# Performance work log

Hardware: AMD Instinct MI355X
Metric: run time of the kernel (lower is better)

The kernel has to match this reference:

```python
import jax, jax.numpy as jnp
import numpy as np

B, H, W, C = 32, 64, 64, 512
NH, WH, WW = 16, 8, 8
SH, SW = 4, 4
FF = 2048
META = 384
A = WH * WW
EPS = 1e-5


def _rel_coords_log():
    # pairwise relative coords in log-space, shape (A*A, 2)
    coords = np.stack(np.meshgrid(np.arange(WH), np.arange(WW), indexing='ij')).reshape(2, -1)
    rel = coords[:, :, None] - coords[:, None, :]
    rel = rel.transpose(1, 2, 0).reshape(-1, 2).astype(np.float32)
    return np.sign(rel) * np.log1p(np.abs(rel))


def _attn_mask():
    # shifted-window attention mask, shape (nW, A, A)
    img = np.zeros((H, W), np.float32)
    cnt = 0
    for hs in (slice(0, -WH), slice(-WH, -SH), slice(-SH, None)):
        for ws in (slice(0, -WW), slice(-WW, -SW), slice(-SW, None)):
            img[hs, ws] = cnt
            cnt += 1
    mw = img.reshape(H // WH, WH, W // WW, WW).transpose(0, 2, 1, 3).reshape(-1, A)
    diff = mw[:, None, :] - mw[:, :, None]
    return np.where(diff != 0, -100.0, 0.0).astype(np.float32)


def setup_inputs():
    key = jax.random.key(0)
    ks = jax.random.split(key, 8)
    s = 0.02
    return {
        'x': jax.random.normal(ks[0], (B, H * W, C), jnp.float32),
        'qkv_w': jax.random.normal(ks[1], (C, 3 * C), jnp.float32) * s,
        'qkv_b': jnp.zeros((3 * C,), jnp.float32),
        'proj_w': jax.random.normal(ks[2], (C, C), jnp.float32) * s,
        'proj_b': jnp.zeros((C,), jnp.float32),
        'tau': jnp.ones((NH,), jnp.float32),
        'meta_w1': jax.random.normal(ks[3], (2, META), jnp.float32) * s,
        'meta_b1': jnp.zeros((META,), jnp.float32),
        'meta_w2': jax.random.normal(ks[4], (META, NH), jnp.float32) * s,
        'meta_b2': jnp.zeros((NH,), jnp.float32),
        'norm1_g': jnp.ones((C,), jnp.float32),
        'norm1_b': jnp.zeros((C,), jnp.float32),
        'norm2_g': jnp.ones((C,), jnp.float32),
        'norm2_b': jnp.zeros((C,), jnp.float32),
        'mlp_w1': jax.random.normal(ks[5], (C, FF), jnp.float32) * s,
        'mlp_b1': jnp.zeros((FF,), jnp.float32),
        'mlp_w2': jax.random.normal(ks[6], (FF, C), jnp.float32) * s,
        'mlp_b2': jnp.zeros((C,), jnp.float32),
    }


def _layernorm(x, g, b):
    mu = x.mean(-1, keepdims=True)
    var = ((x - mu) ** 2).mean(-1, keepdims=True)
    return (x - mu) * jax.lax.rsqrt(var + EPS) * g + b


def reference(x, qkv_w, qkv_b, proj_w, proj_b, tau, meta_w1, meta_b1, meta_w2, meta_b2,
              norm1_g, norm1_b, norm2_g, norm2_b, mlp_w1, mlp_b1, mlp_w2, mlp_b2):
    rel_log = jnp.asarray(_rel_coords_log())
    mask = jnp.asarray(_attn_mask())                 # (nW, A, A)
    nW = mask.shape[0]
    hd = C // NH

    # relative position bias from meta MLP (dropout inactive at eval)
    bias = jax.nn.relu(rel_log @ meta_w1 + meta_b1) @ meta_w2 + meta_b2  # (A*A, NH)
    bias = bias.T.reshape(NH, A, A)

    # cyclic shift + window partition
    xr = x.reshape(B, H, W, C)
    xr = jnp.roll(xr, (-SH, -SW), axis=(1, 2))
    xw = xr.reshape(B, H // WH, WH, W // WW, WW, C).transpose(0, 1, 3, 2, 4, 5)
    xw = xw.reshape(B * nW, A, C)

    qkv = (xw @ qkv_w + qkv_b).reshape(B * nW, A, 3, NH, hd).transpose(2, 0, 3, 1, 4)
    q, k, v = qkv[0], qkv[1], qkv[2]                 # (B*nW, NH, A, hd)

    qn = jnp.linalg.norm(q, axis=-1, keepdims=True)
    kn = jnp.linalg.norm(k, axis=-1, keepdims=True)
    denom = jnp.clip(qn * kn.transpose(0, 1, 3, 2), 1e-6, None)
    attn = jnp.einsum('wnid,wnjd->wnij', q, k) / denom
    attn = attn / jnp.clip(tau, 0.01, None).reshape(1, NH, 1, 1)
    attn = attn + bias[None]
    attn = attn.reshape(B, nW, NH, A, A) + mask[None, :, None]
    attn = jax.nn.softmax(attn.reshape(B * nW, NH, A, A), axis=-1)

    out = jnp.einsum('wnij,wnjd->wnid', attn, v)
    out = out.transpose(0, 2, 1, 3).reshape(B * nW, A, C)
    out = out @ proj_w + proj_b

    # window reverse + reverse shift
    out = out.reshape(B, H // WH, W // WW, WH, WW, C).transpose(0, 1, 3, 2, 4, 5).reshape(B, H, W, C)
    out = jnp.roll(out, (SH, SW), axis=(1, 2)).reshape(B, H * W, C)

    # swin-v2 post-norm residuals
    x = x + _layernorm(out, norm1_g, norm1_b)
    hmid = jax.nn.gelu(x @ mlp_w1 + mlp_b1, approximate=False) @ mlp_w2 + mlp_b2
    x = x + _layernorm(hmid, norm2_g, norm2_b)
    return x
```

## Files before the change

kernel.cpp:

```cpp
#include <hip/hip_runtime.h>

typedef unsigned short u16;
typedef __attribute__((ext_vector_type(8))) short     bf16x8;
typedef __attribute__((ext_vector_type(8))) unsigned short u16x8;
typedef __attribute__((ext_vector_type(4))) unsigned short u16x4;
typedef __attribute__((ext_vector_type(4))) float     f32x4;

#define GADDR(p) ((const __attribute__((address_space(1))) void*)(p))
#define LADDR(p) ((__attribute__((address_space(3))) void*)(p))

__device__ __forceinline__ u16 f2bf(float f) {
  unsigned u = __float_as_uint(f);
  u += 0x7fffu + ((u >> 16) & 1u);
  return (u16)(u >> 16);
}
__device__ __forceinline__ float bf2f(u16 h) {
  return __uint_as_float(((unsigned)h) << 16);
}

__global__ void wt_kernel(const float* __restrict__ w, u16* __restrict__ wt,
                          int K, int N) {
  size_t idx = (size_t)blockIdx.x * 256 + threadIdx.x;
  if (idx >= (size_t)K * N) return;
  int n = (int)(idx / K);
  int k = (int)(idx % K);
  wt[idx] = f2bf(w[(size_t)k * N + n]);
}

__global__ __launch_bounds__(64)
void bias_kernel(const float* __restrict__ w1, const float* __restrict__ b1,
                 const float* __restrict__ w2, const float* __restrict__ b2,
                 float* __restrict__ out) {
  const int p = blockIdx.x;
  const int i = p >> 6, j = p & 63;
  const float d0 = (float)((i >> 3) - (j >> 3));
  const float d1 = (float)((i & 7) - (j & 7));
  const float r0 = copysignf(log1pf(fabsf(d0)), d0);
  const float r1 = copysignf(log1pf(fabsf(d1)), d1);
  float part[16];
#pragma unroll
  for (int h = 0; h < 16; ++h) part[h] = 0.f;
  for (int m = threadIdx.x; m < 384; m += 64) {
    float hv = fmaxf(r0 * w1[m] + r1 * w1[384 + m] + b1[m], 0.f);
#pragma unroll
    for (int h = 0; h < 16; ++h) part[h] += hv * w2[m * 16 + h];
  }
#pragma unroll
  for (int h = 0; h < 16; ++h) {
    float v = part[h];
#pragma unroll
    for (int off = 32; off; off >>= 1) v += __shfl_xor(v, off);
    if (threadIdx.x == 0) out[(size_t)h * 4096 + p] = v + b2[h];
  }
}

__global__ __launch_bounds__(64)
void bias2_kernel(const float* __restrict__ bb, float* __restrict__ b2) {
  const int blk = blockIdx.x;
  const int h = blk >> 4, mi = (blk >> 2) & 3, ni = blk & 3;
  const int lane = threadIdx.x, fr = lane & 15, fq = lane >> 4;
  float4 o;
  o.x = bb[(size_t)h * 4096 + (mi * 16 + fq * 4 + 0) * 64 + ni * 16 + fr];
  o.y = bb[(size_t)h * 4096 + (mi * 16 + fq * 4 + 1) * 64 + ni * 16 + fr];
  o.z = bb[(size_t)h * 4096 + (mi * 16 + fq * 4 + 2) * 64 + ni * 16 + fr];
  o.w = bb[(size_t)h * 4096 + (mi * 16 + fq * 4 + 3) * 64 + ni * 16 + fr];
  ((float4*)b2)[(size_t)blk * 64 + lane] = o;
}

__global__ __launch_bounds__(512)
void partition_kernel(const float* __restrict__ x, u16* __restrict__ xw) {
  const size_t r = (size_t)blockIdx.x * 4 + (threadIdx.x >> 7);
  const int t = threadIdx.x & 127;
  const int w   = (int)(r >> 6);
  const int i   = (int)(r & 63);
  const int b   = w >> 6;
  const int win = w & 63;
  const int hs = (((win >> 3) << 3) + (i >> 3) + 4) & 63;
  const int ws2 = (((win & 7) << 3) + (i & 7) + 4) & 63;
  const float4* src = (const float4*)(x + (((size_t)b << 12) + hs * 64 + ws2) * 512);
  u16* dst = xw + r * 512;
  float4 v = src[t];
  u16x4 o;
  o[0] = f2bf(v.x); o[1] = f2bf(v.y); o[2] = f2bf(v.z); o[3] = f2bf(v.w);
  *(u16x4*)(dst + t * 4) = o;
}

template <int MODE>
__global__ __launch_bounds__(512, 1)
void gemm8(const u16* __restrict__ A, const u16* __restrict__ Wt,
           const float* __restrict__ bias, void* __restrict__ outp,
           int M, int N, int K) {
  __shared__ u16 lds[65536];
  const int t = threadIdx.x;
  const int gx = gridDim.x;
  const int nwg = gx * gridDim.y;
  const int wg = blockIdx.y * gx + blockIdx.x;
  const int swzb = (wg & 7) * (nwg >> 3) + (wg >> 3);
  const int n0 = (swzb % gx) * 256;
  const int m0 = (swzb / gx) * 256;

  const int lane = t & 63;
  const int wid = t >> 6;
  const int wr = (wid >> 2) * 128;
  const int wc = (wid & 3) * 64;
  const int fr = lane & 15, fq = lane >> 4;
  const int c0 = (fq ^ (fr & 7)) * 8;
  const int c1 = ((4 + fq) ^ (fr & 7)) * 8;

  const int tq = t >> 3;
  const int scol = ((t & 7) ^ (tq & 7)) * 8;
  const u16* Asrc = A  + (size_t)(m0 + tq) * K + scol;
  const int rowB = (tq & 31) + ((t >> 8) << 6);
  const u16* Bsrc = Wt + (size_t)(n0 + rowB) * K + scol;
  const int dA = t * 8;
  const int dB = 16384 + ((t >> 8) << 11) + t * 8;

#define SG_A(slot, src, h) do {                                               \
    const int _d = (slot) * 32768 + (h) * 4096 + dA;                          \
    const size_t _k = (size_t)(src) * 64 + (size_t)((h) * 64) * K;            \
    __builtin_amdgcn_global_load_lds(GADDR(Asrc + _k), LADDR(&lds[_d]), 16, 0, 0); \
    __builtin_amdgcn_global_load_lds(GADDR(Asrc + _k + (size_t)128 * K),      \
                                     LADDR(&lds[_d + 8192]), 16, 0, 0);       \
  } while (0)
#define SG_B(slot, src, h) do {                                               \
    const int _d = (slot) * 32768 + (h) * 2048 + dB;                          \
    const size_t _k = (size_t)(src) * 64 + (size_t)((h) * 32) * K;            \
    __builtin_amdgcn_global_load_lds(GADDR(Bsrc + _k), LADDR(&lds[_d]), 16, 0, 0); \
    __builtin_amdgcn_global_load_lds(GADDR(Bsrc + _k + (size_t)128 * K),      \
                                     LADDR(&lds[_d + 8192]), 16, 0, 0);       \
  } while (0)

  f32x4 acc[8][4];
#pragma unroll
  for (int a = 0; a < 8; ++a)
#pragma unroll
    for (int b = 0; b < 4; ++b) acc[a][b] = (f32x4){0.f, 0.f, 0.f, 0.f};

  const int NT = K >> 6;
  SG_A(0, 0, 0); SG_A(0, 0, 1); SG_B(0, 0, 0); SG_B(0, 0, 1);
  SG_A(1, 1, 0); SG_B(1, 1, 0); SG_B(1, 1, 1);
  asm volatile("s_waitcnt vmcnt(6)" ::: "memory");
  __builtin_amdgcn_s_barrier();

#define TILE_BODY(S, SLOT, NSLOT, P0_COND)                                    \
  {                                                                           \
    const u16* la = lds + (SLOT) * 32768;                                     \
    const u16* lb = la + 16384;                                               \
    bf16x8 af[8], bf0[4], bf1[4];                                             \
    _Pragma("unroll")                                                         \
    for (int mi = 0; mi < 4; ++mi) {                                          \
      const int r = (wr + mi * 16 + fr) * 64;                                 \
      af[mi * 2]     = *(const bf16x8*)&la[r + c0];                           \
      af[mi * 2 + 1] = *(const bf16x8*)&la[r + c1];                           \
    }                                                                         \
    _Pragma("unroll")                                                         \
    for (int ni = 0; ni < 2; ++ni) {                                          \
      const int r = (wc + ni * 16 + fr) * 64;                                 \
      bf0[ni * 2]     = *(const bf16x8*)&lb[r + c0];                          \
      bf0[ni * 2 + 1] = *(const bf16x8*)&lb[r + c1];                          \
    }                                                                         \
    if (P0_COND) SG_A(NSLOT, (S) + 1, 1);                                     \
    __builtin_amdgcn_s_barrier();                                             \
    asm volatile("s_waitcnt lgkmcnt(0)" ::: "memory");                        \
    __builtin_amdgcn_sched_barrier(0);                                        \
    __builtin_amdgcn_s_setprio(1);                                            \
    _Pragma("unroll")                                                         \
    for (int mi = 0; mi < 4; ++mi)                                            \
      _Pragma("unroll")                                                       \
      for (int ni = 0; ni < 2; ++ni) {                                        \
        acc[mi][ni] = __builtin_amdgcn_mfma_f32_16x16x32_bf16(                \
            af[mi * 2], bf0[ni * 2], acc[mi][ni], 0, 0, 0);                   \
        acc[mi][ni] = __builtin_amdgcn_mfma_f32_16x16x32_bf16(                \
            af[mi * 2 + 1], bf0[ni * 2 + 1], acc[mi][ni], 0, 0, 0);           \
      }                                                                       \
    __builtin_amdgcn_s_setprio(0);                                            \
    __builtin_amdgcn_s_barrier();                                             \
    _Pragma("unroll")                                                         \
    for (int ni = 0; ni < 2; ++ni) {                                          \
      const int r = (wc + 32 + ni * 16 + fr) * 64;                            \
      bf1[ni * 2]     = *(const bf16x8*)&lb[r + c0];                          \
      bf1[ni * 2 + 1] = *(const bf16x8*)&lb[r + c1];                          \
    }                                                                         \
    if ((S) + 2 < NT) SG_A(SLOT, (S) + 2, 0);                                 \
    __builtin_amdgcn_s_barrier();                                             \
    asm volatile("s_waitcnt lgkmcnt(0)" ::: "memory");                        \
    __builtin_amdgcn_sched_barrier(0);                                        \
    __builtin_amdgcn_s_setprio(1);                                            \
    _Pragma("unroll")                                                         \
    for (int mi = 0; mi < 4; ++mi)                                            \
      _Pragma("unroll")                                                       \
      for (int ni = 0; ni < 2; ++ni) {                                        \
        acc[mi][2 + ni] = __builtin_amdgcn_mfma_f32_16x16x32_bf16(            \
            af[mi * 2], bf1[ni * 2], acc[mi][2 + ni], 0, 0, 0);               \
        acc[mi][2 + ni] = __builtin_amdgcn_mfma_f32_16x16x32_bf16(            \
            af[mi * 2 + 1], bf1[ni * 2 + 1], acc[mi][2 + ni], 0, 0, 0);       \
      }                                                                       \
    __builtin_amdgcn_s_setprio(0);                                            \
    __builtin_amdgcn_s_barrier();                                             \
    _Pragma("unroll")                                                         \
    for (int mi = 0; mi < 4; ++mi) {                                          \
      const int r = (wr + 64 + mi * 16 + fr) * 64;                            \
      af[mi * 2]     = *(const bf16x8*)&la[r + c0];                           \
      af[mi * 2 + 1] = *(const bf16x8*)&la[r + c1];                           \
    }                                                                         \
    if ((S) + 2 < NT) SG_B(SLOT, (S) + 2, 0);                                 \
    __builtin_amdgcn_s_barrier();                                             \
    asm volatile("s_waitcnt lgkmcnt(0)" ::: "memory");                        \
    __builtin_amdgcn_sched_barrier(0);                                        \
    __builtin_amdgcn_s_setprio(1);                                            \
    _Pragma("unroll")                                                         \
    for (int mi = 0; mi < 4; ++mi)                                            \
      _Pragma("unroll")                                                       \
      for (int ni = 0; ni < 2; ++ni) {                                        \
        acc[4 + mi][ni] = __builtin_amdgcn_mfma_f32_16x16x32_bf16(            \
            af[mi * 2], bf0[ni * 2], acc[4 + mi][ni], 0, 0, 0);               \
        acc[4 + mi][ni] = __builtin_amdgcn_mfma_f32_16x16x32_bf16(            \
            af[mi * 2 + 1], bf0[ni * 2 + 1], acc[4 + mi][ni], 0, 0, 0);       \
      }                                                                       \
    __builtin_amdgcn_s_setprio(0);                                            \
    __builtin_amdgcn_s_barrier();                                             \
    if ((S) + 2 < NT) SG_B(SLOT, (S) + 2, 1);                                 \
    __builtin_amdgcn_s_barrier();                                             \
    __builtin_amdgcn_s_setprio(1);                                            \
    _Pragma("unroll")                                                         \
    for (int mi = 0; mi < 4; ++mi)                                            \
      _Pragma("unroll")                                                       \
      for (int ni = 0; ni < 2; ++ni) {                                        \
        acc[4 + mi][2 + ni] = __builtin_amdgcn_mfma_f32_16x16x32_bf16(        \
            af[mi * 2], bf1[ni * 2], acc[4 + mi][2 + ni], 0, 0, 0);           \
        acc[4 + mi][2 + ni] = __builtin_amdgcn_mfma_f32_16x16x32_bf16(        \
            af[mi * 2 + 1], bf1[ni * 2 + 1], acc[4 + mi][2 + ni], 0, 0, 0);   \
      }                                                                       \
    __builtin_amdgcn_s_setprio(0);                                            \
    if ((S) + 2 < NT) asm volatile("s_waitcnt vmcnt(6)" ::: "memory");        \
    else              asm volatile("s_waitcnt vmcnt(0)" ::: "memory");        \
    __builtin_amdgcn_s_barrier();                                             \
  }

  for (int s = 0; s < NT; s += 2) {
    TILE_BODY(s,     0, 1, true);
    TILE_BODY(s + 1, 1, 0, (s + 2 < NT));
  }
#undef TILE_BODY
#undef SG_A
#undef SG_B
  asm volatile("s_waitcnt vmcnt(0)" ::: "memory");
  __syncthreads();

  float bv4[4];
#pragma unroll
  for (int ni = 0; ni < 4; ++ni) bv4[ni] = bias[n0 + wc + ni * 16 + fr];

  u16* uW = &lds[wid * 8192];
  u16* og = (u16*)outp;
#pragma unroll
  for (int mi = 0; mi < 8; ++mi) {
#pragma unroll
    for (int ni = 0; ni < 4; ++ni)
#pragma unroll
      for (int j = 0; j < 4; ++j) {
        float v = acc[mi][ni][j] + bv4[ni];
        if (MODE == 2) {
          const float a2 = v * (1.5957691216f + 0.0713548162f * v * v);
          const float e = __expf(a2);
          v = v * (e * __builtin_amdgcn_rcpf(e + 1.0f));
        }
        uW[(fq * 4 + j) * 64 + ((ni ^ j ^ fq) & 3) * 16 + fr] = f2bf(v);
      }
#pragma unroll
    for (int p = 0; p < 2; ++p) {
      const int r = p * 8 + (lane >> 3);
      const int sg = (((lane & 7) >> 1) ^ (r & 3) ^ ((r >> 2) & 3)) & 3;
      u16x8 v8 = *(const u16x8*)&uW[r * 64 + sg * 16 + (lane & 1) * 8];
      const int row = m0 + wr + mi * 16 + r;
      *(u16x8*)&og[(size_t)row * N + n0 + wc + (lane & 7) * 8] = v8;
    }
  }
}

template <int LNM>
__global__ __launch_bounds__(512, 1)
void gemm_ln(const u16* __restrict__ A, const u16* __restrict__ Wt,
             const float* __restrict__ bias, const u16* __restrict__ residb,
             const float* __restrict__ g, const float* __restrict__ bt,
             float* __restrict__ out1, u16* __restrict__ out1b, int K) {
  __shared__ u16 lds[61440];
  const int t = threadIdx.x;
  const int nwg = gridDim.x;
  const int wg = blockIdx.x;
  const int swz = (wg & 7) * (nwg >> 3) + (wg >> 3);
  const int m0 = swz * 128;

  const int lane = t & 63;
  const int wid = t >> 6;
  const int wc = wid * 64;
  const int fr = lane & 15, fq = lane >> 4;
  const int rx = (fr >> 1) & 3;

  const int srow = t >> 2;
  const int schk = ((t & 3) ^ ((srow >> 1) & 3)) * 8;
  const u16* Ag = A  + (size_t)(m0 + srow) * K + schk;
  const u16* Bg = Wt + (size_t)srow * K + schk;

#define GLSTAGE_A(tile, buf)                                                  \
    __builtin_amdgcn_global_load_lds(GADDR(Ag + (size_t)(tile) * 32),         \
        LADDR(&lds[(buf) * 20480 + t * 8]), 16, 0, 0)
#define GLSTAGE_B(tile, buf, p)                                               \
    __builtin_amdgcn_global_load_lds(                                         \
        GADDR(Bg + (size_t)(p) * 128 * K + (size_t)(tile) * 32),              \
        LADDR(&lds[(buf) * 20480 + 4096 + (p) * 4096 + t * 8]), 16, 0, 0)

  f32x4 acc[8][4];
#pragma unroll
  for (int a = 0; a < 8; ++a)
#pragma unroll
    for (int b = 0; b < 4; ++b) acc[a][b] = (f32x4){0.f, 0.f, 0.f, 0.f};

  const int NT = K >> 5;
  GLSTAGE_A(0, 0);
  GLSTAGE_B(0, 0, 0); GLSTAGE_B(0, 0, 1); GLSTAGE_B(0, 0, 2); GLSTAGE_B(0, 0, 3);
  GLSTAGE_A(1, 1);
  GLSTAGE_B(1, 1, 0); GLSTAGE_B(1, 1, 1); GLSTAGE_B(1, 1, 2); GLSTAGE_B(1, 1, 3);

  int cur = 0;
  for (int u = 0; u < NT; ++u) {
    if (u + 1 < NT) asm volatile("s_waitcnt vmcnt(5)" ::: "memory");
    else            asm volatile("s_waitcnt vmcnt(0)" ::: "memory");
    __builtin_amdgcn_s_barrier();

    const u16* lb = lds + cur * 20480;
    const int stg = (cur == 0) ? 2 : cur - 1;
    bf16x8 bfr[4], af0[4], af1[4];
#pragma unroll
    for (int ni = 0; ni < 4; ++ni)
      bfr[ni] = *(const bf16x8*)&lb[4096 + (wc + ni * 16 + fr) * 32 + (fq ^ rx) * 8];
#pragma unroll
    for (int mi = 0; mi < 4; ++mi)
      af0[mi] = *(const bf16x8*)&lb[(mi * 16 + fr) * 32 + (fq ^ rx) * 8];
    if (u + 2 < NT) {
      GLSTAGE_A(u + 2, stg);
      GLSTAGE_B(u + 2, stg, 0); GLSTAGE_B(u + 2, stg, 1);
    }
#pragma unroll
    for (int mi = 0; mi < 4; ++mi)
      af1[mi] = *(const bf16x8*)&lb[((4 + mi) * 16 + fr) * 32 + (fq ^ rx) * 8];
    if (u + 2 < NT) {
      GLSTAGE_B(u + 2, stg, 2); GLSTAGE_B(u + 2, stg, 3);
    }

    __builtin_amdgcn_s_setprio(1);
#pragma unroll
    for (int mi = 0; mi < 4; ++mi)
#pragma unroll
      for (int ni = 0; ni < 4; ++ni)
        acc[mi][ni] = __builtin_amdgcn_mfma_f32_16x16x32_bf16(
            af0[mi], bfr[ni], acc[mi][ni], 0, 0, 0);
    __builtin_amdgcn_s_setprio(0);
    __builtin_amdgcn_s_setprio(1);
#pragma unroll
    for (int mi = 0; mi < 4; ++mi)
#pragma unroll
      for (int ni = 0; ni < 4; ++ni)
        acc[4 + mi][ni] = __builtin_amdgcn_mfma_f32_16x16x32_bf16(
            af1[mi], bfr[ni], acc[4 + mi][ni], 0, 0, 0);
    __builtin_amdgcn_s_setprio(0);
    cur = (cur == 2) ? 0 : cur + 1;
  }
#undef GLSTAGE_A
#undef GLSTAGE_B

  __syncthreads();
  float bv4[4];
#pragma unroll
  for (int ni = 0; ni < 4; ++ni) bv4[ni] = bias[wc + ni * 16 + fr];
  float4 ga = ((const float4*)g)[lane * 2];
  float4 gb = ((const float4*)g)[lane * 2 + 1];
  float4 ba = ((const float4*)bt)[lane * 2];
  float4 bb = ((const float4*)bt)[lane * 2 + 1];
  const float gv[8] = {ga.x, ga.y, ga.z, ga.w, gb.x, gb.y, gb.z, gb.w};
  const float bv[8] = {ba.x, ba.y, ba.z, ba.w, bb.x, bb.y, bb.z, bb.w};
  float* fLN = (float*)lds;

#pragma unroll
  for (int mi = 0; mi < 8; ++mi) {
#pragma unroll
    for (int ni = 0; ni < 4; ++ni)
#pragma unroll
      for (int j = 0; j < 4; ++j) {
        const int ch = ((wid * 4 + ni) ^ (j << 2) ^ fq) & 31;
        fLN[(fq * 4 + j) * 512 + ch * 16 + fr] = acc[mi][ni][j] + bv4[ni];
      }
    __syncthreads();
#pragma unroll
    for (int rr = 0; rr < 2; ++rr) {
      const int r = wid * 2 + rr;
      const int gci = lane >> 1;
      const int ch = (gci ^ ((r & 3) << 2) ^ (r >> 2)) & 31;
      const int base = r * 512 + ch * 16 + (lane & 1) * 8;
      f32x4 va = *(const f32x4*)&fLN[base];
      f32x4 vb = *(const f32x4*)&fLN[base + 4];
      float v[8] = {va[0], va[1], va[2], va[3], vb[0], vb[1], vb[2], vb[3]};
      float s = 0.f, s2 = 0.f;
#pragma unroll
      for (int e = 0; e < 8; ++e) { s += v[e]; s2 = fmaf(v[e], v[e], s2); }
#pragma unroll
      for (int off = 32; off; off >>= 1) {
        s += __shfl_xor(s, off); s2 += __shfl_xor(s2, off);
      }
      const float mu = s * (1.f / 512.f);
      const float rs = rsqrtf(s2 * (1.f / 512.f) - mu * mu + 1e-5f);
      const int rowg = m0 + mi * 16 + r;
      u16x8 rv8 = *(const u16x8*)(residb + (size_t)rowg * 512 + lane * 8);
      float rv[8];
#pragma unroll
      for (int e = 0; e < 8; ++e) rv[e] = bf2f(rv8[e]);
      float o[8];
#pragma unroll
      for (int e = 0; e < 8; ++e)
        o[e] = rv[e] + (v[e] - mu) * rs * gv[e] + bv[e];
      if (LNM == 0) {
        const int w = rowg >> 6, i = rowg & 63;
        const int b = w >> 6, win = w & 63;
        const int hs = (((win >> 3) << 3) + (i >> 3) + 4) & 63;
        const int ws2 = (((win & 7) << 3) + (i & 7) + 4) & 63;
        const size_t token = ((size_t)b << 12) + hs * 64 + ws2;
        u16x8 ob;
#pragma unroll
        for (int e = 0; e < 8; ++e) ob[e] = f2bf(o[e]);
        *(u16x8*)(out1b + token * 512 + lane * 8) = ob;
      } else {
        float* op = out1 + (size_t)rowg * 512 + lane * 8;
        ((f32x4*)op)[0] = (f32x4){o[0], o[1], o[2], o[3]};
        ((f32x4*)op)[1] = (f32x4){o[4], o[5], o[6], o[7]};
      }
    }
    __syncthreads();
  }
}

__global__ __launch_bounds__(64)
void attn_kernel(const u16* __restrict__ qkv, const float* __restrict__ bias2,
                 const float* __restrict__ tau, u16* __restrict__ ao) {
  const int h = blockIdx.x;
  const int w = blockIdx.y;
  const int lane = threadIdx.x;
  const int fr = lane & 15, fq = lane >> 4;

  __shared__ u16 sh[7424];

  const size_t rowb = ((size_t)w * 64 + lane) * 1536 + (size_t)h * 32;
  u16x8 q8[4], k8[4], v8[4];
#pragma unroll
  for (int u = 0; u < 4; ++u) {
    q8[u] = ((const u16x8*)(qkv + rowb))[u];
    k8[u] = ((const u16x8*)(qkv + rowb + 512))[u];
    v8[u] = ((const u16x8*)(qkv + rowb + 1024))[u];
  }
  float qv[32], kv[32];
  float qn = 0.f, kn = 0.f;
#pragma unroll
  for (int d = 0; d < 32; ++d) {
    qv[d] = bf2f(q8[d >> 3][d & 7]); qn = fmaf(qv[d], qv[d], qn);
    kv[d] = bf2f(k8[d >> 3][d & 7]); kn = fmaf(kv[d], kv[d], kn);
  }
  const float itau = 1.0f / fmaxf(tau[h], 0.01f);
  const float qs = rsqrtf(fmaxf(qn, 1e-24f)) * itau;
  const float ks = rsqrtf(fmaxf(kn, 1e-24f));
#pragma unroll
  for (int u = 0; u < 4; ++u) {
    u16x8 qo, ko;
#pragma unroll
    for (int e = 0; e < 8; ++e) {
      qo[e] = f2bf(qv[u * 8 + e] * qs);
      ko[e] = f2bf(kv[u * 8 + e] * ks);
    }
    *(u16x8*)&sh[lane * 40 + u * 8] = qo;
    *(u16x8*)&sh[2560 + lane * 40 + u * 8] = ko;
  }
#pragma unroll
  for (int d = 0; d < 32; ++d)
    sh[5120 + d * 72 + lane] = v8[d >> 3][d & 7];
  __syncthreads();

  f32x4 acc[4][4];
  const float4* b2 = (const float4*)bias2 + (size_t)h * 1024 + lane;
#pragma unroll
  for (int mi = 0; mi < 4; ++mi)
#pragma unroll
    for (int ni = 0; ni < 4; ++ni) {
      float4 bv = b2[(mi * 4 + ni) * 64];
      acc[mi][ni] = (f32x4){bv.x, bv.y, bv.z, bv.w};
    }
  const int win = w & 63, wh = win >> 3, ww = win & 7;
  if (wh == 7 || ww == 7) {
    int labc[4];
#pragma unroll
    for (int ni = 0; ni < 4; ++ni) {
      const int c = ni * 16 + fr;
      labc[ni] = ((wh == 7) ? (((c >> 3) < 4) ? 1 : 2) : 0) * 3
               + ((ww == 7) ? (((c & 7) < 4) ? 1 : 2) : 0);
    }
#pragma unroll
    for (int mi = 0; mi < 4; ++mi)
#pragma unroll
      for (int j = 0; j < 4; ++j) {
        const int r = mi * 16 + fq * 4 + j;
        const int lr = ((wh == 7) ? (((r >> 3) < 4) ? 1 : 2) : 0) * 3
                     + ((ww == 7) ? (((r & 7) < 4) ? 1 : 2) : 0);
#pragma unroll
        for (int ni = 0; ni < 4; ++ni)
          if (lr != labc[ni]) acc[mi][ni][j] -= 100.f;
      }
  }

  {
    bf16x8 af[4], bf[4];
#pragma unroll
    for (int mi = 0; mi < 4; ++mi)
      af[mi] = *(const bf16x8*)&sh[(mi * 16 + fr) * 40 + fq * 8];
#pragma unroll
    for (int ni = 0; ni < 4; ++ni)
      bf[ni] = *(const bf16x8*)&sh[2560 + (ni * 16 + fr) * 40 + fq * 8];
#pragma unroll
    for (int mi = 0; mi < 4; ++mi)
#pragma unroll
      for (int ni = 0; ni < 4; ++ni)
        acc[mi][ni] = __builtin_amdgcn_mfma_f32_16x16x32_bf16(
            af[mi], bf[ni], acc[mi][ni], 0, 0, 0);
  }

  float lrec[4][4];
#pragma unroll
  for (int mi = 0; mi < 4; ++mi) {
#pragma unroll
    for (int j = 0; j < 4; ++j) {
      float m4 = fmaxf(fmaxf(acc[mi][0][j], acc[mi][1][j]),
                       fmaxf(acc[mi][2][j], acc[mi][3][j]));
#pragma unroll
      for (int mk = 1; mk < 16; mk <<= 1) m4 = fmaxf(m4, __shfl_xor(m4, mk));
      float e0 = __expf(acc[mi][0][j] - m4);
      float e1 = __expf(acc[mi][1][j] - m4);
      float e2 = __expf(acc[mi][2][j] - m4);
      float e3 = __expf(acc[mi][3][j] - m4);
      float s4 = (e0 + e1) + (e2 + e3);
#pragma unroll
      for (int mk = 1; mk < 16; mk <<= 1) s4 += __shfl_xor(s4, mk);
      lrec[mi][j] = __builtin_amdgcn_rcpf(s4);
      const int r = mi * 16 + fq * 4 + j;
      sh[r * 72 +  0 + fr] = f2bf(e0);
      sh[r * 72 + 16 + fr] = f2bf(e1);
      sh[r * 72 + 32 + fr] = f2bf(e2);
      sh[r * 72 + 48 + fr] = f2bf(e3);
    }
  }
  __syncthreads();

  f32x4 acc2[4][2];
#pragma unroll
  for (int mi = 0; mi < 4; ++mi)
#pragma unroll
    for (int n2 = 0; n2 < 2; ++n2) acc2[mi][n2] = (f32x4){0.f, 0.f, 0.f, 0.f};
#pragma unroll
  for (int kk = 0; kk < 2; ++kk) {
    bf16x8 pf[4], vf[2];
#pragma unroll
    for (int mi = 0; mi < 4; ++mi)
      pf[mi] = *(const bf16x8*)&sh[(mi * 16 + fr) * 72 + kk * 32 + fq * 8];
#pragma unroll
    for (int n2 = 0; n2 < 2; ++n2)
      vf[n2] = *(const bf16x8*)&sh[5120 + (n2 * 16 + fr) * 72 + kk * 32 + fq * 8];
#pragma unroll
    for (int mi = 0; mi < 4; ++mi)
#pragma unroll
      for (int n2 = 0; n2 < 2; ++n2)
        acc2[mi][n2] = __builtin_amdgcn_mfma_f32_16x16x32_bf16(
            pf[mi], vf[n2], acc2[mi][n2], 0, 0, 0);
  }

  u16* op = ao + ((size_t)w * 64) * 512 + (size_t)h * 32;
#pragma unroll
  for (int mi = 0; mi < 4; ++mi)
#pragma unroll
    for (int j = 0; j < 4; ++j) {
      const int r = mi * 16 + fq * 4 + j;
      const float sc = lrec[mi][j];
      op[(size_t)r * 512 +  0 + fr] = f2bf(acc2[mi][0][j] * sc);
      op[(size_t)r * 512 + 16 + fr] = f2bf(acc2[mi][1][j] * sc);
    }
}

extern "C" void kernel_launch(void* const* d_in, const int* in_sizes, int n_in,
                              void* d_out, int out_size, void* d_ws, size_t ws_size,
                              hipStream_t stream) {
  const float* x      = (const float*)d_in[0];
  const float* qkv_w  = (const float*)d_in[1];
  const float* qkv_b  = (const float*)d_in[2];
  const float* proj_w = (const float*)d_in[3];
  const float* proj_b = (const float*)d_in[4];
  const float* tau    = (const float*)d_in[5];
  const float* mw1    = (const float*)d_in[6];
  const float* mb1    = (const float*)d_in[7];
  const float* mw2    = (const float*)d_in[8];
  const float* mb2    = (const float*)d_in[9];
  const float* n1g    = (const float*)d_in[10];
  const float* n1b    = (const float*)d_in[11];
  const float* n2g    = (const float*)d_in[12];
  const float* n2b    = (const float*)d_in[13];
  const float* mlp_w1 = (const float*)d_in[14];
  const float* mlp_b1 = (const float*)d_in[15];
  const float* mlp_w2 = (const float*)d_in[16];
  const float* mlp_b2 = (const float*)d_in[17];

  char* ws = (char*)d_ws;
  u16*   WQKVT  = (u16*)  (ws + 0);
  u16*   WPROJT = (u16*)  (ws + 1572864);
  u16*   WM1T   = (u16*)  (ws + 2097152);
  u16*   WM2T   = (u16*)  (ws + 4194304);
  float* BIASB  = (float*)(ws + 6291456);
  float* BIAS2  = (float*)(ws + 6553600);
  const size_t CH0 = 8388608;

  int CB = 32;
  while (CB > 1 && CH0 + (size_t)CB * 29360128ull > ws_size) CB >>= 1;
  const int NCH = 32 / CB;
  const size_t Mc = (size_t)CB * 4096;

  u16*   XW   = (u16*)  (ws + CH0);
  u16*   QKV  = (u16*)  (ws + CH0 + Mc * 1024);
  u16*   HBUF = QKV;
  u16*   AO   = (u16*)  (ws + CH0 + Mc * 5120);
  u16*   X1B  = (u16*)  (ws + CH0 + Mc * 6144);

  wt_kernel<<<(512 * 1536 + 255) / 256, 256, 0, stream>>>(qkv_w, WQKVT, 512, 1536);
  wt_kernel<<<(512 * 512 + 255) / 256, 256, 0, stream>>>(proj_w, WPROJT, 512, 512);
  wt_kernel<<<(512 * 2048 + 255) / 256, 256, 0, stream>>>(mlp_w1, WM1T, 512, 2048);
  wt_kernel<<<(2048 * 512 + 255) / 256, 256, 0, stream>>>(mlp_w2, WM2T, 2048, 512);
  bias_kernel<<<4096, 64, 0, stream>>>(mw1, mb1, mw2, mb2, BIASB);
  bias2_kernel<<<256, 64, 0, stream>>>(BIASB, BIAS2);

  const unsigned MB = (unsigned)(Mc / 256);
  const unsigned LB = (unsigned)(Mc / 128);

  for (int c = 0; c < NCH; ++c) {
    const float* xc = x + (size_t)c * Mc * 512;
    float* oc = (float*)d_out + (size_t)c * Mc * 512;

    partition_kernel<<<(unsigned)(Mc / 4), 512, 0, stream>>>(xc, XW);
    gemm8<0><<<dim3(6, MB), 512, 0, stream>>>(XW, WQKVT, qkv_b, QKV,
                                              (int)Mc, 1536, 512);
    attn_kernel<<<dim3(16, CB * 64), 64, 0, stream>>>(QKV, BIAS2, tau, AO);
    gemm_ln<0><<<LB, 512, 0, stream>>>(AO, WPROJT, proj_b, XW, n1g, n1b,
                                       nullptr, X1B, 512);
    gemm8<2><<<dim3(8, MB), 512, 0, stream>>>(X1B, WM1T, mlp_b1, HBUF,
                                              (int)Mc, 2048, 512);
    gemm_ln<1><<<LB, 512, 0, stream>>>(HBUF, WM2T, mlp_b2, X1B, n2g, n2b,
                                       oc, nullptr, 2048);
  }
}
```

Measured before the change: 1.424 ms.

## Split gemm8 block tile across 16 waves with 64x64 per-wave tiles

```diff
diff --git a/kernel.cpp b/kernel.cpp
--- a/kernel.cpp
+++ b/kernel.cpp
@@ -86,7 +86,7 @@
 }
 
 template <int MODE>
-__global__ __launch_bounds__(512, 1)
+__global__ __launch_bounds__(1024, 4)
 void gemm8(const u16* __restrict__ A, const u16* __restrict__ Wt,
            const float* __restrict__ bias, void* __restrict__ outp,
            int M, int N, int K) {
@@ -101,71 +101,67 @@
 
   const int lane = t & 63;
   const int wid = t >> 6;
-  const int wr = (wid >> 2) * 128;
+  const int wr = (wid >> 2) * 64;
   const int wc = (wid & 3) * 64;
   const int fr = lane & 15, fq = lane >> 4;
   const int c0 = (fq ^ (fr & 7)) * 8;
   const int c1 = ((4 + fq) ^ (fr & 7)) * 8;
+  const int aS = (wid >> 2) * 32;
+  const int bS = (wid & 3) * 32;
 
   const int tq = t >> 3;
+  const int arow = (tq >> 5) * 64 + (tq & 31);
   const int scol = ((t & 7) ^ (tq & 7)) * 8;
-  const u16* Asrc = A  + (size_t)(m0 + tq) * K + scol;
-  const int rowB = (tq & 31) + ((t >> 8) << 6);
-  const u16* Bsrc = Wt + (size_t)(n0 + rowB) * K + scol;
-  const int dA = t * 8;
-  const int dB = 16384 + ((t >> 8) << 11) + t * 8;
-
-#define SG_A(slot, src, h) do {                                               \
-    const int _d = (slot) * 32768 + (h) * 4096 + dA;                          \
-    const size_t _k = (size_t)(src) * 64 + (size_t)((h) * 64) * K;            \
-    __builtin_amdgcn_global_load_lds(GADDR(Asrc + _k), LADDR(&lds[_d]), 16, 0, 0); \
-    __builtin_amdgcn_global_load_lds(GADDR(Asrc + _k + (size_t)128 * K),      \
-                                     LADDR(&lds[_d + 8192]), 16, 0, 0);       \
-  } while (0)
-#define SG_B(slot, src, h) do {                                               \
-    const int _d = (slot) * 32768 + (h) * 2048 + dB;                          \
-    const size_t _k = (size_t)(src) * 64 + (size_t)((h) * 32) * K;            \
-    __builtin_amdgcn_global_load_lds(GADDR(Bsrc + _k), LADDR(&lds[_d]), 16, 0, 0); \
-    __builtin_amdgcn_global_load_lds(GADDR(Bsrc + _k + (size_t)128 * K),      \
-                                     LADDR(&lds[_d + 8192]), 16, 0, 0);       \
-  } while (0)
-
-  f32x4 acc[8][4];
-#pragma unroll
-  for (int a = 0; a < 8; ++a)
+  const u16* Asrc = A  + (size_t)(m0 + arow) * K + scol;
+  const u16* Bsrc = Wt + (size_t)(n0 + arow) * K + scol;
+  const int dD = t * 8;
+
+#define SG_A(slot, src, h)                                                    \
+    __builtin_amdgcn_global_load_lds(                                         \
+        GADDR(Asrc + (size_t)(src) * 64 + (size_t)((h) * 32) * K),            \
+        LADDR(&lds[(slot) * 32768 + (h) * 8192 + dD]), 16, 0, 0)
+#define SG_B(slot, src, h)                                                    \
+    __builtin_amdgcn_global_load_lds(                                         \
+        GADDR(Bsrc + (size_t)(src) * 64 + (size_t)((h) * 32) * K),            \
+        LADDR(&lds[(slot) * 32768 + 16384 + (h) * 8192 + dD]), 16, 0, 0)
+
+  f32x4 acc[4][4];
+#pragma unroll
+  for (int a = 0; a < 4; ++a)
 #pragma unroll
     for (int b = 0; b < 4; ++b) acc[a][b] = (f32x4){0.f, 0.f, 0.f, 0.f};
 
   const int NT = K >> 6;
   SG_A(0, 0, 0); SG_A(0, 0, 1); SG_B(0, 0, 0); SG_B(0, 0, 1);
   SG_A(1, 1, 0); SG_B(1, 1, 0); SG_B(1, 1, 1);
-  asm volatile("s_waitcnt vmcnt(6)" ::: "memory");
+  asm volatile("s_waitcnt vmcnt(3)" ::: "memory");
   __builtin_amdgcn_s_barrier();
 
-#define TILE_BODY(S, SLOT, NSLOT, P0_COND)                                    \
+#define TILE_BODY(S, SLOT, NSLOT, C1, C2)                                     \
   {                                                                           \
     const u16* la = lds + (SLOT) * 32768;                                     \
     const u16* lb = la + 16384;                                               \
-    bf16x8 af[8], bf0[4], bf1[4];                                             \
-    _Pragma("unroll")                                                         \
-    for (int mi = 0; mi < 4; ++mi) {                                          \
-      const int r = (wr + mi * 16 + fr) * 64;                                 \
+    bf16x8 af[4], bf0[4], bf1[4];                                             \
+                            \
+    _Pragma("unroll")                                                         \
+    for (int mi = 0; mi < 2; ++mi) {                                          \
+      const int r = (aS + mi * 16 + fr) * 64;                                 \
       af[mi * 2]     = *(const bf16x8*)&la[r + c0];                           \
       af[mi * 2 + 1] = *(const bf16x8*)&la[r + c1];                           \
     }                                                                         \
     _Pragma("unroll")                                                         \
     for (int ni = 0; ni < 2; ++ni) {                                          \
-      const int r = (wc + ni * 16 + fr) * 64;                                 \
+      const int r = (bS + ni * 16 + fr) * 64;                                 \
       bf0[ni * 2]     = *(const bf16x8*)&lb[r + c0];                          \
       bf0[ni * 2 + 1] = *(const bf16x8*)&lb[r + c1];                          \
     }                                                                         \
-    if (P0_COND) SG_A(NSLOT, (S) + 1, 1);                                     \
+    if (C1) SG_A(NSLOT, (S) + 1, 1);                                          \
     __builtin_amdgcn_s_barrier();                                             \
     asm volatile("s_waitcnt lgkmcnt(0)" ::: "memory");                        \
     __builtin_amdgcn_sched_barrier(0);                                        \
     __builtin_amdgcn_s_setprio(1);                                            \
     _Pragma("unroll")                                                         \
-    for (int mi = 0; mi < 4; ++mi)                                            \
+    for (int mi = 0; mi < 2; ++mi)                                            \
       _Pragma("unroll")                                                       \
       for (int ni = 0; ni < 2; ++ni) {                                        \
         acc[mi][ni] = __builtin_amdgcn_mfma_f32_16x16x32_bf16(                \
@@ -175,19 +171,20 @@
       }                                                                       \
     __builtin_amdgcn_s_setprio(0);                                            \
     __builtin_amdgcn_s_barrier();                                             \
+                                            \
     _Pragma("unroll")                                                         \
     for (int ni = 0; ni < 2; ++ni) {                                          \
-      const int r = (wc + 32 + ni * 16 + fr) * 64;                            \
+      const int r = 8192 + (bS + ni * 16 + fr) * 64;                          \
       bf1[ni * 2]     = *(const bf16x8*)&lb[r + c0];                          \
       bf1[ni * 2 + 1] = *(const bf16x8*)&lb[r + c1];                          \
     }                                                                         \
-    if ((S) + 2 < NT) SG_A(SLOT, (S) + 2, 0);                                 \
+    if (C2) SG_A(SLOT, (S) + 2, 0);                                           \
     __builtin_amdgcn_s_barrier();                                             \
     asm volatile("s_waitcnt lgkmcnt(0)" ::: "memory");                        \
     __builtin_amdgcn_sched_barrier(0);                                        \
     __builtin_amdgcn_s_setprio(1);                                            \
     _Pragma("unroll")                                                         \
-    for (int mi = 0; mi < 4; ++mi)                                            \
+    for (int mi = 0; mi < 2; ++mi)                                            \
       _Pragma("unroll")                                                       \
       for (int ni = 0; ni < 2; ++ni) {                                        \
         acc[mi][2 + ni] = __builtin_amdgcn_mfma_f32_16x16x32_bf16(            \
@@ -197,49 +194,61 @@
       }                                                                       \
     __builtin_amdgcn_s_setprio(0);                                            \
     __builtin_amdgcn_s_barrier();                                             \
-    _Pragma("unroll")                                                         \
-    for (int mi = 0; mi < 4; ++mi) {                                          \
-      const int r = (wr + 64 + mi * 16 + fr) * 64;                            \
+                            \
+    _Pragma("unroll")                                                         \
+    for (int mi = 0; mi < 2; ++mi) {                                          \
+      const int r = 8192 + (aS + mi * 16 + fr) * 64;                          \
       af[mi * 2]     = *(const bf16x8*)&la[r + c0];                           \
       af[mi * 2 + 1] = *(const bf16x8*)&la[r + c1];                           \
     }                                                                         \
-    if ((S) + 2 < NT) SG_B(SLOT, (S) + 2, 0);                                 \
+    _Pragma("unroll")                                                         \
+    for (int ni = 0; ni < 2; ++ni) {                                          \
+      const int r = (bS + ni * 16 + fr) * 64;                                 \
+      bf0[ni * 2]     = *(const bf16x8*)&lb[r + c0];                          \
+      bf0[ni * 2 + 1] = *(const bf16x8*)&lb[r + c1];                          \
+    }                                                                         \
+    _Pragma("unroll")                                                         \
+    for (int ni = 0; ni < 2; ++ni) {                                          \
+      const int r = 8192 + (bS + ni * 16 + fr) * 64;                          \
+      bf1[ni * 2]     = *(const bf16x8*)&lb[r + c0];                          \
+      bf1[ni * 2 + 1] = *(const bf16x8*)&lb[r + c1];                          \
+    }                                                                         \
     __builtin_amdgcn_s_barrier();                                             \
     asm volatile("s_waitcnt lgkmcnt(0)" ::: "memory");                        \
     __builtin_amdgcn_sched_barrier(0);                                        \
     __builtin_amdgcn_s_setprio(1);                                            \
     _Pragma("unroll")                                                         \
-    for (int mi = 0; mi < 4; ++mi)                                            \
+    for (int mi = 0; mi < 2; ++mi)                                            \
       _Pragma("unroll")                                                       \
       for (int ni = 0; ni < 2; ++ni) {                                        \
-        acc[4 + mi][ni] = __builtin_amdgcn_mfma_f32_16x16x32_bf16(            \
-            af[mi * 2], bf0[ni * 2], acc[4 + mi][ni], 0, 0, 0);               \
-        acc[4 + mi][ni] = __builtin_amdgcn_mfma_f32_16x16x32_bf16(            \
-            af[mi * 2 + 1], bf0[ni * 2 + 1], acc[4 + mi][ni], 0, 0, 0);       \
+        acc[2 + mi][ni] = __builtin_amdgcn_mfma_f32_16x16x32_bf16(            \
+            af[mi * 2], bf0[ni * 2], acc[2 + mi][ni], 0, 0, 0);               \
+        acc[2 + mi][ni] = __builtin_amdgcn_mfma_f32_16x16x32_bf16(            \
+            af[mi * 2 + 1], bf0[ni * 2 + 1], acc[2 + mi][ni], 0, 0, 0);       \
       }                                                                       \
     __builtin_amdgcn_s_setprio(0);                                            \
     __builtin_amdgcn_s_barrier();                                             \
-    if ((S) + 2 < NT) SG_B(SLOT, (S) + 2, 1);                                 \
-    __builtin_amdgcn_s_barrier();                                             \
+            \
+    if (C2) { SG_B(SLOT, (S) + 2, 0); SG_B(SLOT, (S) + 2, 1); }               \
     __builtin_amdgcn_s_setprio(1);                                            \
     _Pragma("unroll")                                                         \
-    for (int mi = 0; mi < 4; ++mi)                                            \
+    for (int mi = 0; mi < 2; ++mi)                                            \
       _Pragma("unroll")                                                       \
       for (int ni = 0; ni < 2; ++ni) {                                        \
-        acc[4 + mi][2 + ni] = __builtin_amdgcn_mfma_f32_16x16x32_bf16(        \
-            af[mi * 2], bf1[ni * 2], acc[4 + mi][2 + ni], 0, 0, 0);           \
-        acc[4 + mi][2 + ni] = __builtin_amdgcn_mfma_f32_16x16x32_bf16(        \
-            af[mi * 2 + 1], bf1[ni * 2 + 1], acc[4 + mi][2 + ni], 0, 0, 0);   \
+        acc[2 + mi][2 + ni] = __builtin_amdgcn_mfma_f32_16x16x32_bf16(        \
+            af[mi * 2], bf1[ni * 2], acc[2 + mi][2 + ni], 0, 0, 0);           \
+        acc[2 + mi][2 + ni] = __builtin_amdgcn_mfma_f32_16x16x32_bf16(        \
+            af[mi * 2 + 1], bf1[ni * 2 + 1], acc[2 + mi][2 + ni], 0, 0, 0);   \
       }                                                                       \
     __builtin_amdgcn_s_setprio(0);                                            \
-    if ((S) + 2 < NT) asm volatile("s_waitcnt vmcnt(6)" ::: "memory");        \
-    else              asm volatile("s_waitcnt vmcnt(0)" ::: "memory");        \
+    if (C2) asm volatile("s_waitcnt vmcnt(3)" ::: "memory");                  \
+    else    asm volatile("s_waitcnt vmcnt(0)" ::: "memory");                  \
     __builtin_amdgcn_s_barrier();                                             \
   }
 
   for (int s = 0; s < NT; s += 2) {
-    TILE_BODY(s,     0, 1, true);
-    TILE_BODY(s + 1, 1, 0, (s + 2 < NT));
+    TILE_BODY(s,     0, 1, true,         (s + 2 < NT));
+    TILE_BODY(s + 1, 1, 0, (s + 2 < NT), (s + 3 < NT));
   }
 #undef TILE_BODY
 #undef SG_A
@@ -251,10 +260,10 @@
 #pragma unroll
   for (int ni = 0; ni < 4; ++ni) bv4[ni] = bias[n0 + wc + ni * 16 + fr];
 
-  u16* uW = &lds[wid * 8192];
+  u16* uW = &lds[wid * 4096];
   u16* og = (u16*)outp;
 #pragma unroll
-  for (int mi = 0; mi < 8; ++mi) {
+  for (int mi = 0; mi < 4; ++mi) {
 #pragma unroll
     for (int ni = 0; ni < 4; ++ni)
 #pragma unroll
@@ -646,13 +655,13 @@
     float* oc = (float*)d_out + (size_t)c * Mc * 512;
 
     partition_kernel<<<(unsigned)(Mc / 4), 512, 0, stream>>>(xc, XW);
-    gemm8<0><<<dim3(6, MB), 512, 0, stream>>>(XW, WQKVT, qkv_b, QKV,
-                                              (int)Mc, 1536, 512);
+    gemm8<0><<<dim3(6, MB), 1024, 0, stream>>>(XW, WQKVT, qkv_b, QKV,
+                                               (int)Mc, 1536, 512);
     attn_kernel<<<dim3(16, CB * 64), 64, 0, stream>>>(QKV, BIAS2, tau, AO);
     gemm_ln<0><<<LB, 512, 0, stream>>>(AO, WPROJT, proj_b, XW, n1g, n1b,
                                        nullptr, X1B, 512);
-    gemm8<2><<<dim3(8, MB), 512, 0, stream>>>(X1B, WM1T, mlp_b1, HBUF,
-                                              (int)Mc, 2048, 512);
+    gemm8<2><<<dim3(8, MB), 1024, 0, stream>>>(X1B, WM1T, mlp_b1, HBUF,
+                                               (int)Mc, 2048, 512);
     gemm_ln<1><<<LB, 512, 0, stream>>>(HBUF, WM2T, mlp_b2, X1B, n2g, n2b,
                                        oc, nullptr, 2048);
   }
```

Result: slower. 2.058 ms (+44.5%).
